# Optimization experiments

Measured on AMD Instinct MI355X. Metric: run time of the kernel, lower is better.

Reference implementation:

```python
import jax, jax.numpy as jnp
import numpy as np

NEG_INF = float('-inf')


def _apply_top_k_top_p(logits, k, p):
    """Sort-based top-k + top-p filtering, faithful to vLLM's _apply_top_k_top_p.

    logits: [B, V] (already temperature-scaled)
    k: [B] int32 top-k per row
    p: [B] float32 top-p per row
    """
    V = logits.shape[-1]
    idx = jnp.argsort(logits, axis=-1)                      # ascending order indices [B, V]
    logits_sort = jnp.take_along_axis(logits, idx, axis=-1)  # ascending sorted values
    # top-k: threshold is the (V-k)-th smallest value; everything strictly below -> -inf
    thresh = jnp.take_along_axis(logits_sort, (V - k.astype(jnp.int32))[:, None], axis=-1)
    logits_sort = jnp.where(logits_sort < thresh, NEG_INF, logits_sort)
    # top-p: mask the low-probability tail whose cumulative mass <= 1 - p
    probs_sum = jnp.cumsum(jax.nn.softmax(logits_sort, axis=-1), axis=-1)
    tp_mask = probs_sum <= (1.0 - p)[:, None]
    tp_mask = tp_mask.at[:, -1].set(False)  # always keep the max-logit token
    logits_sort = jnp.where(tp_mask, NEG_INF, logits_sort)
    # scatter back to original vocab order via inverse permutation
    inv = jnp.argsort(idx, axis=-1)
    return jnp.take_along_axis(logits_sort, inv, axis=-1)


def setup_inputs() -> dict:
    key = jax.random.key(0)
    k1, k2, k3, k4 = jax.random.split(key, 4)
    B, V = 256, 128000
    logits = jax.random.normal(k1, (B, V), dtype=jnp.float32)
    temperature = jax.random.uniform(k2, (B,), dtype=jnp.float32, minval=0.5, maxval=1.5)
    k = jax.random.randint(k3, (B,), 16, 1024, dtype=jnp.int32)
    p = jax.random.uniform(k4, (B,), dtype=jnp.float32, minval=0.9, maxval=1.0)
    return {"logits": logits, "temperature": temperature, "k": k, "p": p,
            "max_num_logprobs": 5}


def reference(logits, temperature, k, p, max_num_logprobs):
    # temperature scale
    x = logits / temperature[:, None]
    # sort-based top-k / top-p filtering
    x = _apply_top_k_top_p(x, k, p)
    # multinomial sample from softmax(x)  (categorical over filtered logits)
    sampled = jax.random.categorical(jax.random.key(42), x, axis=-1)  # [B]
    # logprobs of the filtered distribution + top-k logprob extraction
    logprobs = jax.nn.log_softmax(x, axis=-1)                          # [B, V]
    topk_lp, topk_idx = jax.lax.top_k(logprobs, max_num_logprobs)      # [B, K]
    sampled_lp = jnp.take_along_axis(logprobs, sampled[:, None], axis=-1)  # [B, 1]
    lp_out = jnp.concatenate([topk_lp, sampled_lp], axis=-1)               # [B, K+1]
    idx_out = jnp.concatenate([topk_idx.astype(jnp.int32),
                               sampled[:, None].astype(jnp.int32)], axis=-1)
    return sampled.astype(jnp.int32), lp_out, idx_out
```

## Files before the change

### kernel.cpp

```cpp
#include <hip/hip_runtime.h>
#include <stdint.h>

#define BLOCK 1024
#define NW (BLOCK / 64)
#define CAP 8192

__device__ __forceinline__ unsigned fkey(float x) {
  unsigned u = __float_as_uint(x);
  return (u & 0x80000000u) ? ~u : (u | 0x80000000u);
}
__device__ __forceinline__ float funkey(unsigned k) {
  return __uint_as_float((k & 0x80000000u) ? (k & 0x7FFFFFFFu) : ~k);
}

__device__ __forceinline__ void threefry(unsigned x0, unsigned x1, unsigned& o0, unsigned& o1) {
  const unsigned ks0 = 0u, ks1 = 42u, ks2 = 0u ^ 42u ^ 0x1BD11BDAu;
  x0 += ks0; x1 += ks1;
#define TF_ROUND(r) { x0 += x1; x1 = (x1 << (r)) | (x1 >> (32 - (r))); x1 ^= x0; }
  TF_ROUND(13) TF_ROUND(15) TF_ROUND(26) TF_ROUND(6)
  x0 += ks1; x1 += ks2 + 1u;
  TF_ROUND(17) TF_ROUND(29) TF_ROUND(16) TF_ROUND(24)
  x0 += ks2; x1 += ks0 + 2u;
  TF_ROUND(13) TF_ROUND(15) TF_ROUND(26) TF_ROUND(6)
  x0 += ks0; x1 += ks1 + 3u;
  TF_ROUND(17) TF_ROUND(29) TF_ROUND(16) TF_ROUND(24)
  x0 += ks1; x1 += ks2 + 4u;
  TF_ROUND(13) TF_ROUND(15) TF_ROUND(26) TF_ROUND(6)
  x0 += ks2; x1 += ks0 + 5u;
#undef TF_ROUND
  o0 = x0; o1 = x1;
}

__device__ __forceinline__ float gumbel_from_bits(unsigned bits) {
  const float tiny = 1.17549435e-38f;
  float f = __uint_as_float((bits >> 9) | 0x3F800000u) - 1.0f;
  float u = fmaxf(tiny, f * (1.0f - tiny) + tiny);
  return -logf(-logf(u));
}

__device__ __forceinline__ float gumbel_noise(unsigned long long j) {
  unsigned o0, o1;
  threefry((unsigned)(j >> 32), (unsigned)j, o0, o1);
  return gumbel_from_bits(o0 ^ o1);
}

#define T5_INSERT(t5, key) do {                                             \
    if ((key) > (t5)[4]) {                                                  \
      (t5)[4] = (key);                                                      \
      unsigned long long _tmp;                                              \
      if ((t5)[4] > (t5)[3]) { _tmp=(t5)[4]; (t5)[4]=(t5)[3]; (t5)[3]=_tmp; }\
      if ((t5)[3] > (t5)[2]) { _tmp=(t5)[3]; (t5)[3]=(t5)[2]; (t5)[2]=_tmp; }\
      if ((t5)[2] > (t5)[1]) { _tmp=(t5)[2]; (t5)[2]=(t5)[1]; (t5)[1]=_tmp; }\
      if ((t5)[1] > (t5)[0]) { _tmp=(t5)[1]; (t5)[1]=(t5)[0]; (t5)[0]=_tmp; }\
    }                                                                       \
  } while (0)

extern "C" __global__ void __launch_bounds__(BLOCK)
sampler_kernel(const float* __restrict__ logits,
               const float* __restrict__ temperature,
               const int* __restrict__ topk,
               const float* __restrict__ topp,
               float* __restrict__ out, int B, int V)
{
  __shared__ unsigned long long cand[CAP];
  __shared__ float aux[CAP];
  __shared__ float redf[NW];
  __shared__ float redf2[NW];
  __shared__ float redf3[NW];
  __shared__ unsigned long long redu[NW];
  __shared__ unsigned long long t5red[NW][5];
  __shared__ int   sh_n0;
  __shared__ float sh_t0, sh_sigma;
  __shared__ int   sh_pos0, sh_pos1;
  __shared__ float sh_S1, sh_S2;
  __shared__ unsigned long long sh_best;

  const int b = blockIdx.x;
  const int tid = threadIdx.x;
  const int lane = tid & 63;
  const int wid = tid >> 6;
  const float t = temperature[b];
  const int kk = topk[b];
  const float p = topp[b];
  const float* __restrict__ row = logits + (size_t)b * V;
  const float4* __restrict__ row4 = (const float4*)row;
  const int N4 = V >> 2;
  const float inv = 1.0f / t;

  {
    float ls = 0.f, ls2 = 0.f;
#pragma unroll
    for (int j = 0; j < 4; j++) {
      int i4 = tid + j * 8192;
      if (i4 < N4) {
        float4 s = row4[i4];
        float a0 = s.x * inv, a1 = s.y * inv, a2 = s.z * inv, a3 = s.w * inv;
        ls += (a0 + a1) + (a2 + a3);
        ls2 += (a0 * a0 + a1 * a1) + (a2 * a2 + a3 * a3);
      }
    }
#pragma unroll
    for (int o = 32; o; o >>= 1) { ls += __shfl_down(ls, o); ls2 += __shfl_down(ls2, o); }
    if (lane == 0) { redf2[wid] = ls; redf3[wid] = ls2; }
    __syncthreads();
    if (tid == 0) {
      float s = 0.f, s2 = 0.f;
      for (int i = 0; i < NW; i++) { s += redf2[i]; s2 += redf3[i]; }
      const float ns = 16384.f;
      float mu = s / ns;
      float var = fmaxf(s2 / ns - mu * mu, 0.f);
      float sigma = sqrtf(var);
      if (!(sigma > 1e-20f)) sigma = 1.f;
      int target = min(4000, max(1344, kk + (kk >> 2) + 192));
      float q = (float)target / (float)V;
      float tt = sqrtf(-2.f * logf(q));
      float z = tt - (2.30753f + 0.27061f * tt) / (1.f + 0.99229f * tt + 0.04481f * tt * tt);
      sh_sigma = sigma;
      sh_t0 = mu + sigma * (z - 0.10f);
      sh_n0 = 0;
    }
    __syncthreads();
  }

  unsigned long long t5[5];
  {
    const unsigned long long kinit = ((unsigned long long)fkey(-INFINITY)) << 32;
    t5[0] = t5[1] = t5[2] = t5[3] = t5[4] = kinit;
  }
  float t5min = -INFINITY;
  int n0 = 0;
  {
    const float thr = sh_t0;
    for (int i4 = tid; i4 < N4; i4 += BLOCK) {
      float4 xv = row4[i4];
      float x0 = xv.x * inv, x1 = xv.y * inv, x2 = xv.z * inv, x3 = xv.w * inv;
      const int vb = i4 << 2;
      if (x0 >= t5min) { unsigned long long key = ((unsigned long long)fkey(x0) << 32) | (0xFFFFFFFFu - (unsigned)(vb + 0)); T5_INSERT(t5, key); t5min = funkey((unsigned)(t5[4] >> 32)); }
      if (x1 >= t5min) { unsigned long long key = ((unsigned long long)fkey(x1) << 32) | (0xFFFFFFFFu - (unsigned)(vb + 1)); T5_INSERT(t5, key); t5min = funkey((unsigned)(t5[4] >> 32)); }
      if (x2 >= t5min) { unsigned long long key = ((unsigned long long)fkey(x2) << 32) | (0xFFFFFFFFu - (unsigned)(vb + 2)); T5_INSERT(t5, key); t5min = funkey((unsigned)(t5[4] >> 32)); }
      if (x3 >= t5min) { unsigned long long key = ((unsigned long long)fkey(x3) << 32) | (0xFFFFFFFFu - (unsigned)(vb + 3)); T5_INSERT(t5, key); t5min = funkey((unsigned)(t5[4] >> 32)); }
      bool p0 = (x0 >= thr), p1 = (x1 >= thr), p2 = (x2 >= thr), p3 = (x3 >= thr);
      int cnt = (int)p0 + (int)p1 + (int)p2 + (int)p3;
      if (cnt) {
        int base = atomicAdd(&sh_n0, cnt);
        if (p0 && base < CAP) { cand[base++] = ((unsigned long long)fkey(x0) << 32) | (unsigned)(vb + 0); }
        if (p1 && base < CAP) { cand[base++] = ((unsigned long long)fkey(x1) << 32) | (unsigned)(vb + 1); }
        if (p2 && base < CAP) { cand[base++] = ((unsigned long long)fkey(x2) << 32) | (unsigned)(vb + 2); }
        if (p3 && base < CAP) { cand[base++] = ((unsigned long long)fkey(x3) << 32) | (unsigned)(vb + 3); }
      }
    }
    __syncthreads();
    n0 = sh_n0;
  }

  for (int attempt = 1; attempt < 8 && (n0 < kk || n0 > CAP); ++attempt) {
    if (tid == 0) {
      if (n0 < kk) sh_t0 -= 0.5f * sh_sigma;
      else         sh_t0 += 0.25f * sh_sigma;
      sh_n0 = 0;
    }
    __syncthreads();
    const float thr = sh_t0;
    for (int i4 = tid; i4 < N4; i4 += BLOCK) {
      float4 xv = row4[i4];
      float x0 = xv.x * inv, x1 = xv.y * inv, x2 = xv.z * inv, x3 = xv.w * inv;
      const int vb = i4 << 2;
      bool p0 = (x0 >= thr), p1 = (x1 >= thr), p2 = (x2 >= thr), p3 = (x3 >= thr);
      int cnt = (int)p0 + (int)p1 + (int)p2 + (int)p3;
      if (cnt) {
        int base = atomicAdd(&sh_n0, cnt);
        if (p0 && base < CAP) { cand[base++] = ((unsigned long long)fkey(x0) << 32) | (unsigned)(vb + 0); }
        if (p1 && base < CAP) { cand[base++] = ((unsigned long long)fkey(x1) << 32) | (unsigned)(vb + 1); }
        if (p2 && base < CAP) { cand[base++] = ((unsigned long long)fkey(x2) << 32) | (unsigned)(vb + 2); }
        if (p3 && base < CAP) { cand[base++] = ((unsigned long long)fkey(x3) << 32) | (unsigned)(vb + 3); }
      }
    }
    __syncthreads();
    n0 = sh_n0;
  }
  if (n0 > CAP) n0 = CAP;

  {
#pragma unroll
    for (int off = 32; off; off >>= 1) {
      unsigned long long o0 = __shfl_down(t5[0], off);
      unsigned long long o1 = __shfl_down(t5[1], off);
      unsigned long long o2 = __shfl_down(t5[2], off);
      unsigned long long o3 = __shfl_down(t5[3], off);
      unsigned long long o4 = __shfl_down(t5[4], off);
      T5_INSERT(t5, o0); T5_INSERT(t5, o1); T5_INSERT(t5, o2);
      T5_INSERT(t5, o3); T5_INSERT(t5, o4);
    }
    if (lane == 0) {
      t5red[wid][0] = t5[0]; t5red[wid][1] = t5[1]; t5red[wid][2] = t5[2];
      t5red[wid][3] = t5[3]; t5red[wid][4] = t5[4];
    }
  }
  __syncthreads();

  if (n0 < 1) {
    if (tid == 0) {
      out[b] = 0.f;
      for (int j = 0; j < 6; j++) { out[B + b * 6 + j] = 0.f; out[B + B * 6 + b * 6 + j] = 0.f; }
    }
    return;
  }

  int n = 1; while (n < n0) n <<= 1;
  if (n < 2) n = 2;
  for (int i = n0 + tid; i < n; i += BLOCK) cand[i] = 0xFFFFFFFFFFFFFFFFull;
  __syncthreads();
  for (int sz = 2; sz <= n; sz <<= 1) {
    for (int st = sz >> 1; st > 0; st >>= 1) {
      for (int i = tid; i < n; i += BLOCK) {
        int j = i ^ st;
        if (j > i) {
          unsigned long long a = cand[i], c = cand[j];
          bool up = ((i & sz) == 0);
          if ((a > c) == up) { cand[i] = c; cand[j] = a; }
        }
      }
      __syncthreads();
    }
  }

  const float M = funkey((unsigned)(cand[n0 - 1] >> 32));

  if (tid == 0) {
    int kc = min(kk, n0);
    unsigned tk = (unsigned)(cand[n0 - kc] >> 32);
    int lo = 0, hi = n0 - kc;
    while (lo < hi) { int mid = (lo + hi) >> 1;
      if ((unsigned)(cand[mid] >> 32) >= tk) hi = mid; else lo = mid + 1; }
    sh_pos0 = lo;
  }
  __syncthreads();
  const int pos0 = sh_pos0;

  for (int i = tid; i < n0; i += BLOCK) {
    float v = funkey((unsigned)(cand[i] >> 32));
    aux[i] = (i >= pos0) ? expf(v - M) : 0.f;
  }
  __syncthreads();
  {
    float sloc = 0.f;
    for (int i = tid; i < n0; i += BLOCK) sloc += aux[i];
#pragma unroll
    for (int o = 32; o; o >>= 1) sloc += __shfl_down(sloc, o);
    if (lane == 0) redf[wid] = sloc;
    __syncthreads();
    if (tid == 0) { float s = 0.f; for (int i = 0; i < NW; i++) s += redf[i]; sh_S1 = s; }
    __syncthreads();
  }
  const float S1 = sh_S1;

  const int C = (n0 + BLOCK - 1) / BLOCK;
  const int beg = tid * C, endp = min(beg + C, n0);
  float sp = 0.f;
  for (int i = beg; i < endp; i++) sp += aux[i] / S1;
  float ws = sp;
#pragma unroll
  for (int off = 1; off < 64; off <<= 1) {
    float v = __shfl_up(ws, off);
    if (lane >= off) ws += v;
  }
  if (lane == 63) redf[wid] = ws;
  __syncthreads();
  if (tid < NW) {
    float v = redf[tid];
#pragma unroll
    for (int off = 1; off < NW; off <<= 1) {
      float u = __shfl_up(v, off);
      if (tid >= off) v += u;
    }
    redf[tid] = v;
  }
  __syncthreads();
  {
    float wbase = (wid > 0) ? redf[wid - 1] : 0.f;
    float run = wbase + (ws - sp);
    for (int i = beg; i < endp; i++) { run += aux[i] / S1; aux[i] = run; }
  }
  __syncthreads();

  const float cutoff = 1.0f - p;
  if (tid == 0) {
    int lo = pos0, hi = n0 - 1;
    while (lo < hi) { int mid = (lo + hi) >> 1;
      if (aux[mid] > cutoff) hi = mid; else lo = mid + 1; }
    sh_pos1 = lo;
  }
  __syncthreads();
  const int pos1 = sh_pos1;

  {
    float sloc = 0.f;
    for (int i = pos1 + tid; i < n0; i += BLOCK) {
      float v = funkey((unsigned)(cand[i] >> 32));
      sloc += expf(v - M);
    }
#pragma unroll
    for (int o = 32; o; o >>= 1) sloc += __shfl_down(sloc, o);
    if (lane == 0) redf2[wid] = sloc;
    __syncthreads();
    if (tid == 0) { float s = 0.f; for (int i = 0; i < NW; i++) s += redf2[i]; sh_S2 = s; }
    __syncthreads();
  }

  unsigned long long best = 0ull;
  for (int i = pos1 + tid; i < n0; i += BLOCK) {
    unsigned idx = (unsigned)(cand[i] & 0xFFFFFFFFull);
    unsigned long long j = (unsigned long long)b * (unsigned long long)V + idx;
    float g = gumbel_noise(j);
    float v = funkey((unsigned)(cand[i] >> 32));
    float sc = v + g;
    unsigned long long pk =
        ((unsigned long long)fkey(sc) << 32) | (unsigned)(0xFFFFFFFFu - (unsigned)i);
    if (pk > best) best = pk;
  }
#pragma unroll
  for (int o = 32; o; o >>= 1) {
    unsigned long long o2 = __shfl_down(best, o);
    if (o2 > best) best = o2;
  }
  if (lane == 0) redu[wid] = best;
  __syncthreads();
  if (tid == 0) {
    unsigned long long bb = 0ull;
    for (int i = 0; i < NW; i++) if (redu[i] > bb) bb = redu[i];
    sh_best = bb;
  }
  __syncthreads();

  if (tid == 0) {
    const float lse = logf(sh_S2);
    int bi = (int)(0xFFFFFFFFu - (unsigned)(sh_best & 0xFFFFFFFFull));
    unsigned sidx = (unsigned)(cand[bi] & 0xFFFFFFFFull);
    float sval = funkey((unsigned)(cand[bi] >> 32));

    unsigned long long f5[5] = {0ull, 0ull, 0ull, 0ull, 0ull};
    for (int w = 0; w < NW; w++) {
      unsigned long long k0 = t5red[w][0], k1 = t5red[w][1], k2 = t5red[w][2],
                         k3 = t5red[w][3], k4 = t5red[w][4];
      T5_INSERT(f5, k0); T5_INSERT(f5, k1); T5_INSERT(f5, k2);
      T5_INSERT(f5, k3); T5_INSERT(f5, k4);
    }

    out[b] = (float)sidx;
    float* lpout = out + B + b * 6;
    float* idout = out + B + B * 6 + b * 6;
    for (int jj = 0; jj < 5; jj++) {
      unsigned long long key = f5[jj];
      float v = funkey((unsigned)(key >> 32));
      unsigned idx = 0xFFFFFFFFu - (unsigned)(key & 0xFFFFFFFFull);
      lpout[jj] = (v - M) - lse;
      idout[jj] = (float)idx;
    }
    lpout[5] = (sval - M) - lse;
    idout[5] = (float)sidx;
  }
}

extern "C" void kernel_launch(void* const* d_in, const int* in_sizes, int n_in,
                              void* d_out, int out_size, void* d_ws, size_t ws_size,
                              hipStream_t stream) {
  const float* logits = (const float*)d_in[0];
  const float* temp   = (const float*)d_in[1];
  const int*   k      = (const int*)d_in[2];
  const float* p      = (const float*)d_in[3];
  float* out = (float*)d_out;
  const int B = in_sizes[1];
  const int V = in_sizes[0] / in_sizes[1];
  hipLaunchKernelGGL(sampler_kernel, dim3(B), dim3(BLOCK), 0, stream,
                     logits, temp, k, p, out, B, V);
}
```

Before: 268.4 us.

## Move top-5 tracking to candidate set, shrink candidate cap, warp-aggregate atomics

Per-element top-5 insertion is removed from the full-vocabulary scan. It is now computed over the sorted candidate buffer after the bitonic sort. The candidate capacity and threshold target are halved, which shrinks the sort. The first scan processes two float4s per thread with a wavefront prefix sum and a single atomic per wave, and compares raw logits against an untempered threshold, scaling only the stored candidates. The softmax and cumsum loops now start at pos0, which skips candidates below the top-k cut. The risk is that the smaller target causes more retries when the estimated threshold misses. The threshold statistics are now computed on unscaled logits, which is consistent only because temperature is positive.

Result: faster. 247.5 us (-7.8%).

```diff
diff --git a/kernel.cpp b/kernel.cpp
--- a/kernel.cpp
+++ b/kernel.cpp
@@ -3,7 +3,7 @@
 
 #define BLOCK 1024
 #define NW (BLOCK / 64)
-#define CAP 8192
+#define CAP 4096
 
 __device__ __forceinline__ unsigned fkey(float x) {
   unsigned u = __float_as_uint(x);
@@ -94,9 +94,8 @@
       int i4 = tid + j * 8192;
       if (i4 < N4) {
         float4 s = row4[i4];
-        float a0 = s.x * inv, a1 = s.y * inv, a2 = s.z * inv, a3 = s.w * inv;
-        ls += (a0 + a1) + (a2 + a3);
-        ls2 += (a0 * a0 + a1 * a1) + (a2 * a2 + a3 * a3);
+        ls  += (s.x + s.y) + (s.z + s.w);
+        ls2 += (s.x * s.x + s.y * s.y) + (s.z * s.z + s.w * s.w);
       }
     }
 #pragma unroll
@@ -111,7 +110,7 @@
       float var = fmaxf(s2 / ns - mu * mu, 0.f);
       float sigma = sqrtf(var);
       if (!(sigma > 1e-20f)) sigma = 1.f;
-      int target = min(4000, max(1344, kk + (kk >> 2) + 192));
+      int target = min(2800, max(kk + (kk >> 2) + 128, 512));
       float q = (float)target / (float)V;
       float tt = sqrtf(-2.f * logf(q));
       float z = tt - (2.30753f + 0.27061f * tt) / (1.f + 0.99229f * tt + 0.04481f * tt * tt);
@@ -122,31 +121,41 @@
     __syncthreads();
   }
 
-  unsigned long long t5[5];
-  {
-    const unsigned long long kinit = ((unsigned long long)fkey(-INFINITY)) << 32;
-    t5[0] = t5[1] = t5[2] = t5[3] = t5[4] = kinit;
-  }
-  float t5min = -INFINITY;
   int n0 = 0;
   {
     const float thr = sh_t0;
-    for (int i4 = tid; i4 < N4; i4 += BLOCK) {
-      float4 xv = row4[i4];
-      float x0 = xv.x * inv, x1 = xv.y * inv, x2 = xv.z * inv, x3 = xv.w * inv;
-      const int vb = i4 << 2;
-      if (x0 >= t5min) { unsigned long long key = ((unsigned long long)fkey(x0) << 32) | (0xFFFFFFFFu - (unsigned)(vb + 0)); T5_INSERT(t5, key); t5min = funkey((unsigned)(t5[4] >> 32)); }
-      if (x1 >= t5min) { unsigned long long key = ((unsigned long long)fkey(x1) << 32) | (0xFFFFFFFFu - (unsigned)(vb + 1)); T5_INSERT(t5, key); t5min = funkey((unsigned)(t5[4] >> 32)); }
-      if (x2 >= t5min) { unsigned long long key = ((unsigned long long)fkey(x2) << 32) | (0xFFFFFFFFu - (unsigned)(vb + 2)); T5_INSERT(t5, key); t5min = funkey((unsigned)(t5[4] >> 32)); }
-      if (x3 >= t5min) { unsigned long long key = ((unsigned long long)fkey(x3) << 32) | (0xFFFFFFFFu - (unsigned)(vb + 3)); T5_INSERT(t5, key); t5min = funkey((unsigned)(t5[4] >> 32)); }
-      bool p0 = (x0 >= thr), p1 = (x1 >= thr), p2 = (x2 >= thr), p3 = (x3 >= thr);
-      int cnt = (int)p0 + (int)p1 + (int)p2 + (int)p3;
-      if (cnt) {
-        int base = atomicAdd(&sh_n0, cnt);
-        if (p0 && base < CAP) { cand[base++] = ((unsigned long long)fkey(x0) << 32) | (unsigned)(vb + 0); }
-        if (p1 && base < CAP) { cand[base++] = ((unsigned long long)fkey(x1) << 32) | (unsigned)(vb + 1); }
-        if (p2 && base < CAP) { cand[base++] = ((unsigned long long)fkey(x2) << 32) | (unsigned)(vb + 2); }
-        if (p3 && base < CAP) { cand[base++] = ((unsigned long long)fkey(x3) << 32) | (unsigned)(vb + 3); }
+    for (int i4 = tid; i4 < N4; i4 += 2 * BLOCK) {
+      float4 A = row4[i4];
+      int ib = i4 + BLOCK;
+      bool hb = (ib < N4);
+      if (!hb) ib = i4;
+      float4 Bv = row4[ib];
+      bool a0 = A.x >= thr, a1 = A.y >= thr, a2 = A.z >= thr, a3 = A.w >= thr;
+      bool b0 = hb && (Bv.x >= thr), b1 = hb && (Bv.y >= thr),
+           b2 = hb && (Bv.z >= thr), b3 = hb && (Bv.w >= thr);
+      int cnt = (int)a0 + (int)a1 + (int)a2 + (int)a3
+              + (int)b0 + (int)b1 + (int)b2 + (int)b3;
+      int incl = cnt;
+#pragma unroll
+      for (int off = 1; off < 64; off <<= 1) {
+        int v = __shfl_up(incl, off);
+        if (lane >= off) incl += v;
+      }
+      int tot = __shfl(incl, 63);
+      if (tot) {
+        int base = 0;
+        if (lane == 63) base = atomicAdd(&sh_n0, tot);
+        base = __shfl(base, 63);
+        int mb = base + incl - cnt;
+        const int va = i4 << 2, vb = ib << 2;
+        if (a0) { if (mb < CAP) cand[mb] = ((unsigned long long)fkey(A.x * inv) << 32) | (unsigned)(va + 0); mb++; }
+        if (a1) { if (mb < CAP) cand[mb] = ((unsigned long long)fkey(A.y * inv) << 32) | (unsigned)(va + 1); mb++; }
+        if (a2) { if (mb < CAP) cand[mb] = ((unsigned long long)fkey(A.z * inv) << 32) | (unsigned)(va + 2); mb++; }
+        if (a3) { if (mb < CAP) cand[mb] = ((unsigned long long)fkey(A.w * inv) << 32) | (unsigned)(va + 3); mb++; }
+        if (b0) { if (mb < CAP) cand[mb] = ((unsigned long long)fkey(Bv.x * inv) << 32) | (unsigned)(vb + 0); mb++; }
+        if (b1) { if (mb < CAP) cand[mb] = ((unsigned long long)fkey(Bv.y * inv) << 32) | (unsigned)(vb + 1); mb++; }
+        if (b2) { if (mb < CAP) cand[mb] = ((unsigned long long)fkey(Bv.z * inv) << 32) | (unsigned)(vb + 2); mb++; }
+        if (b3) { if (mb < CAP) cand[mb] = ((unsigned long long)fkey(Bv.w * inv) << 32) | (unsigned)(vb + 3); mb++; }
       }
     }
     __syncthreads();
@@ -163,40 +172,21 @@
     const float thr = sh_t0;
     for (int i4 = tid; i4 < N4; i4 += BLOCK) {
       float4 xv = row4[i4];
-      float x0 = xv.x * inv, x1 = xv.y * inv, x2 = xv.z * inv, x3 = xv.w * inv;
-      const int vb = i4 << 2;
-      bool p0 = (x0 >= thr), p1 = (x1 >= thr), p2 = (x2 >= thr), p3 = (x3 >= thr);
+      bool p0 = xv.x >= thr, p1 = xv.y >= thr, p2 = xv.z >= thr, p3 = xv.w >= thr;
       int cnt = (int)p0 + (int)p1 + (int)p2 + (int)p3;
       if (cnt) {
         int base = atomicAdd(&sh_n0, cnt);
-        if (p0 && base < CAP) { cand[base++] = ((unsigned long long)fkey(x0) << 32) | (unsigned)(vb + 0); }
-        if (p1 && base < CAP) { cand[base++] = ((unsigned long long)fkey(x1) << 32) | (unsigned)(vb + 1); }
-        if (p2 && base < CAP) { cand[base++] = ((unsigned long long)fkey(x2) << 32) | (unsigned)(vb + 2); }
-        if (p3 && base < CAP) { cand[base++] = ((unsigned long long)fkey(x3) << 32) | (unsigned)(vb + 3); }
+        const int vbb = i4 << 2;
+        if (p0) { if (base < CAP) cand[base] = ((unsigned long long)fkey(xv.x * inv) << 32) | (unsigned)(vbb + 0); base++; }
+        if (p1) { if (base < CAP) cand[base] = ((unsigned long long)fkey(xv.y * inv) << 32) | (unsigned)(vbb + 1); base++; }
+        if (p2) { if (base < CAP) cand[base] = ((unsigned long long)fkey(xv.z * inv) << 32) | (unsigned)(vbb + 2); base++; }
+        if (p3) { if (base < CAP) cand[base] = ((unsigned long long)fkey(xv.w * inv) << 32) | (unsigned)(vbb + 3); base++; }
       }
     }
     __syncthreads();
     n0 = sh_n0;
   }
   if (n0 > CAP) n0 = CAP;
-
-  {
-#pragma unroll
-    for (int off = 32; off; off >>= 1) {
-      unsigned long long o0 = __shfl_down(t5[0], off);
-      unsigned long long o1 = __shfl_down(t5[1], off);
-      unsigned long long o2 = __shfl_down(t5[2], off);
-      unsigned long long o3 = __shfl_down(t5[3], off);
-      unsigned long long o4 = __shfl_down(t5[4], off);
-      T5_INSERT(t5, o0); T5_INSERT(t5, o1); T5_INSERT(t5, o2);
-      T5_INSERT(t5, o3); T5_INSERT(t5, o4);
-    }
-    if (lane == 0) {
-      t5red[wid][0] = t5[0]; t5red[wid][1] = t5[1]; t5red[wid][2] = t5[2];
-      t5red[wid][3] = t5[3]; t5red[wid][4] = t5[4];
-    }
-  }
-  __syncthreads();
 
   if (n0 < 1) {
     if (tid == 0) {
@@ -226,6 +216,30 @@
 
   const float M = funkey((unsigned)(cand[n0 - 1] >> 32));
 
+  {
+    unsigned long long t5[5] = {0ull, 0ull, 0ull, 0ull, 0ull};
+    for (int i = tid; i < n0; i += BLOCK) {
+      unsigned long long ck = cand[i];
+      unsigned long long tk = (ck & 0xFFFFFFFF00000000ull) |
+                              (unsigned)(0xFFFFFFFFu - (unsigned)(ck & 0xFFFFFFFFull));
+      T5_INSERT(t5, tk);
+    }
+#pragma unroll
+    for (int off = 32; off; off >>= 1) {
+      unsigned long long o0 = __shfl_down(t5[0], off);
+      unsigned long long o1 = __shfl_down(t5[1], off);
+      unsigned long long o2 = __shfl_down(t5[2], off);
+      unsigned long long o3 = __shfl_down(t5[3], off);
+      unsigned long long o4 = __shfl_down(t5[4], off);
+      T5_INSERT(t5, o0); T5_INSERT(t5, o1); T5_INSERT(t5, o2);
+      T5_INSERT(t5, o3); T5_INSERT(t5, o4);
+    }
+    if (lane == 0) {
+      t5red[wid][0] = t5[0]; t5red[wid][1] = t5[1]; t5red[wid][2] = t5[2];
+      t5red[wid][3] = t5[3]; t5red[wid][4] = t5[4];
+    }
+  }
+
   if (tid == 0) {
     int kc = min(kk, n0);
     unsigned tk = (unsigned)(cand[n0 - kc] >> 32);
@@ -237,14 +251,14 @@
   __syncthreads();
   const int pos0 = sh_pos0;
 
-  for (int i = tid; i < n0; i += BLOCK) {
+  for (int i = pos0 + tid; i < n0; i += BLOCK) {
     float v = funkey((unsigned)(cand[i] >> 32));
-    aux[i] = (i >= pos0) ? expf(v - M) : 0.f;
+    aux[i] = expf(v - M);
   }
   __syncthreads();
   {
     float sloc = 0.f;
-    for (int i = tid; i < n0; i += BLOCK) sloc += aux[i];
+    for (int i = pos0 + tid; i < n0; i += BLOCK) sloc += aux[i];
 #pragma unroll
     for (int o = 32; o; o >>= 1) sloc += __shfl_down(sloc, o);
     if (lane == 0) redf[wid] = sloc;
@@ -254,8 +268,10 @@
   }
   const float S1 = sh_S1;
 
-  const int C = (n0 + BLOCK - 1) / BLOCK;
-  const int beg = tid * C, endp = min(beg + C, n0);
+  const int m = n0 - pos0;
+  const int C = (m + BLOCK - 1) / BLOCK;
+  const int beg = pos0 + tid * C;
+  const int endp = min(beg + C, n0);
   float sp = 0.f;
   for (int i = beg; i < endp; i++) sp += aux[i] / S1;
   float ws = sp;
```
